# Performance work log

Measured on AMD Instinct MI355X. Metric: run time of the kernel, lower is better.

Reference implementation:

```python
import jax, jax.numpy as jnp
import numpy as np

D_MODEL, N_HEAD, D_HEAD, N_LAYERS, D_FF = 1024, 16, 64, 6, 4096
SEQ_LEN, MEM_LEN, BATCH, CLAMP_LEN = 512, 128, 4, 512
LN_EPS = 1e-5


def layernorm(x, g, b):
    mu = jnp.mean(x, axis=-1, keepdims=True)
    var = jnp.var(x, axis=-1, keepdims=True)
    return (x - mu) * jax.lax.rsqrt(var + LN_EPS) * g + b


def rel_shift(x):
    # x: (qlen, rlen, B, H) -> Transformer-XL relative shift
    q, r, b, n = x.shape
    zp = jnp.zeros((q, 1, b, n), x.dtype)
    xp = jnp.concatenate([zp, x], axis=1).reshape(r + 1, q, b, n)
    return xp[1:].reshape(q, r, b, n)


def pos_embedding(klen):
    # sinusoidal embedding on positions klen-1 .. 0, clamped at CLAMP_LEN
    pos = jnp.arange(klen - 1, -1, -1.0, dtype=jnp.float32)
    pos = jnp.minimum(pos, float(CLAMP_LEN))
    inv_freq = 1.0 / (10000.0 ** (jnp.arange(0.0, D_MODEL, 2.0) / D_MODEL))
    sin_inp = pos[:, None] * inv_freq[None, :]  # (klen, D/2)
    return jnp.concatenate([jnp.sin(sin_inp), jnp.cos(sin_inp)], axis=-1)  # (klen, D)


def setup_inputs() -> dict:
    key = jax.random.key(0)
    ks = jax.random.split(key, 16)
    s = 0.02
    return {
        "inputs": jax.random.normal(ks[0], (SEQ_LEN, BATCH, D_MODEL), jnp.float32),
        "mems": jax.random.normal(ks[1], (N_LAYERS, MEM_LEN, BATCH, D_MODEL), jnp.float32),
        "r_w_bias": jax.random.normal(ks[2], (N_HEAD, D_HEAD), jnp.float32) * s,
        "r_r_bias": jax.random.normal(ks[3], (N_HEAD, D_HEAD), jnp.float32) * s,
        "qkv_w": jax.random.normal(ks[4], (N_LAYERS, 3 * N_HEAD * D_HEAD, D_MODEL), jnp.float32) * s,
        "r_w": jax.random.normal(ks[5], (N_LAYERS, N_HEAD * D_HEAD, D_MODEL), jnp.float32) * s,
        "o_w": jax.random.normal(ks[6], (N_LAYERS, D_MODEL, N_HEAD * D_HEAD), jnp.float32) * s,
        "ln1_g": jnp.ones((N_LAYERS, D_MODEL), jnp.float32),
        "ln1_b": jnp.zeros((N_LAYERS, D_MODEL), jnp.float32),
        "ff_w1": jax.random.normal(ks[7], (N_LAYERS, D_FF, D_MODEL), jnp.float32) * s,
        "ff_b1": jnp.zeros((N_LAYERS, D_FF), jnp.float32),
        "ff_w2": jax.random.normal(ks[8], (N_LAYERS, D_MODEL, D_FF), jnp.float32) * s,
        "ff_b2": jnp.zeros((N_LAYERS, D_MODEL), jnp.float32),
        "ln2_g": jnp.ones((N_LAYERS, D_MODEL), jnp.float32),
        "ln2_b": jnp.zeros((N_LAYERS, D_MODEL), jnp.float32),
        "fin_g": jnp.ones((D_MODEL,), jnp.float32),
        "fin_b": jnp.zeros((D_MODEL,), jnp.float32),
    }


def reference(inputs, mems, r_w_bias, r_r_bias, qkv_w, r_w, o_w,
              ln1_g, ln1_b, ff_w1, ff_b1, ff_w2, ff_b2, ln2_g, ln2_b,
              fin_g, fin_b):
    qlen, bsz, _ = inputs.shape
    mlen = mems.shape[1]
    klen = mlen + qlen
    scale = 1.0 / np.sqrt(D_HEAD)

    pos_emb = pos_embedding(klen)  # (klen, D)
    # causal mask with memory: True = masked
    attn_mask = jnp.triu(jnp.ones((qlen, klen), bool), k=1 + mlen)

    x = inputs  # (T, B, D)
    for l in range(N_LAYERS):
        # ---- relative multi-head attention (pre_lnorm) ----
        cat = jnp.concatenate([mems[l], x], axis=0)           # (klen, B, D)
        h = layernorm(cat, ln1_g[l], ln1_b[l])
        w_heads = jnp.einsum('kbd,ed->kbe', h, qkv_w[l])      # (klen, B, 3HD)
        r_head_k = jnp.einsum('kd,ed->ke', pos_emb, r_w[l])   # (klen, HD)
        hd = N_HEAD * D_HEAD
        q = w_heads[-qlen:, :, :hd].reshape(qlen, bsz, N_HEAD, D_HEAD)
        k = w_heads[:, :, hd:2 * hd].reshape(klen, bsz, N_HEAD, D_HEAD)
        v = w_heads[:, :, 2 * hd:].reshape(klen, bsz, N_HEAD, D_HEAD)
        r_head_k = r_head_k.reshape(klen, N_HEAD, D_HEAD)

        AC = jnp.einsum('ibnd,jbnd->ijbn', q + r_w_bias, k)
        BD = rel_shift(jnp.einsum('ibnd,jnd->ijbn', q + r_r_bias, r_head_k))
        score = (AC + BD) * scale                              # (q, k, B, H)
        score = jnp.where(attn_mask[:, :, None, None], -jnp.inf, score)
        prob = jax.nn.softmax(score, axis=1)
        attn_vec = jnp.einsum('ijbn,jbnd->ibnd', prob, v).reshape(qlen, bsz, hd)
        attn_out = jnp.einsum('ibe,de->ibd', attn_vec, o_w[l])
        x = x + attn_out

        # ---- position-wise FFN (pre_lnorm) ----
        hf = layernorm(x, ln2_g[l], ln2_b[l])
        hf = jax.nn.relu(jnp.einsum('ibd,fd->ibf', hf, ff_w1[l]) + ff_b1[l])
        hf = jnp.einsum('ibf,df->ibd', hf, ff_w2[l]) + ff_b2[l]
        x = x + hf

    return layernorm(x, fin_g, fin_b)
```

## Files before the change

kernel.cpp:

```cpp
#include <hip/hip_runtime.h>
#include <math.h>
#include <stdint.h>

#define DM    1024
#define NH    16
#define DH    64
#define NL    6
#define DFF   4096
#define QLEN  512
#define MLEN  128
#define B_    4
#define KL    640
#define CLAMP 512
#define EPS   1e-5f

typedef _Float16 f16x8 __attribute__((ext_vector_type(8)));
typedef _Float16 f16x4 __attribute__((ext_vector_type(4)));
typedef float    f32x4 __attribute__((ext_vector_type(4)));

__device__ __forceinline__ void gload16(const void* g, void* l) {
  __builtin_amdgcn_global_load_lds(
      (const __attribute__((address_space(1))) void*)g,
      (__attribute__((address_space(3))) void*)l, 16, 0, 0);
}

__device__ __forceinline__ float block_sum(float v, float* sm4) {
#pragma unroll
  for (int o = 32; o > 0; o >>= 1) v += __shfl_down(v, o, 64);
  int lane = threadIdx.x & 63, wid = threadIdx.x >> 6;
  if (lane == 0) sm4[wid] = v;
  __syncthreads();
  float r = sm4[0] + sm4[1] + sm4[2] + sm4[3];
  __syncthreads();
  return r;
}

__global__ __launch_bounds__(256) void pos_emb_kernel(_Float16* __restrict__ pe) {
  int p = blockIdx.x;
  float pos = fminf((float)(KL - 1 - p), (float)CLAMP);
  for (int f = threadIdx.x; f < 512; f += 256) {
    float inv = powf(10000.0f, -(float)f * (1.0f / 512.0f));
    float a = pos * inv;
    pe[(size_t)p * DM + f]       = (_Float16)sinf(a);
    pe[(size_t)p * DM + 512 + f] = (_Float16)cosf(a);
  }
}

__global__ __launch_bounds__(256) void cast_w_kernel(
    const float* __restrict__ s0, const float* __restrict__ s1,
    const float* __restrict__ s2, const float* __restrict__ s3,
    const float* __restrict__ s4, _Float16* __restrict__ dst) {
  size_t i = ((size_t)blockIdx.x * 256 + threadIdx.x) * 4;
  const float* src; size_t off;
  if (i < 3145728)      { src = s0; off = 0; }
  else if (i < 4194304) { src = s1; off = 3145728; }
  else if (i < 5242880) { src = s2; off = 4194304; }
  else if (i < 9437184) { src = s3; off = 5242880; }
  else                  { src = s4; off = 9437184; }
  float4 v = *(const float4*)(src + (i - off));
  f16x4 o = { (_Float16)v.x, (_Float16)v.y, (_Float16)v.z, (_Float16)v.w };
  *(f16x4*)(dst + i) = o;
}

template <int OUTF16>
__global__ __launch_bounds__(256) void ln_kernel(
    const float* __restrict__ src0, const float* __restrict__ src1,
    const float* __restrict__ g, const float* __restrict__ b,
    float* __restrict__ outf, _Float16* __restrict__ outh, int rows0) {
  __shared__ float sm4[4];
  int row = blockIdx.x;
  const float* src = (row < rows0) ? (src0 + (size_t)row * DM)
                                   : (src1 + (size_t)(row - rows0) * DM);
  float4 v = ((const float4*)src)[threadIdx.x];
  float mean = block_sum(v.x + v.y + v.z + v.w, sm4) * (1.0f / DM);
  float dx = v.x - mean, dy = v.y - mean, dz = v.z - mean, dw = v.w - mean;
  float var = block_sum(dx * dx + dy * dy + dz * dz + dw * dw, sm4) * (1.0f / DM);
  float rstd = rsqrtf(var + EPS);
  float4 gg = ((const float4*)g)[threadIdx.x];
  float4 bb = ((const float4*)b)[threadIdx.x];
  float ox = dx * rstd * gg.x + bb.x;
  float oy = dy * rstd * gg.y + bb.y;
  float oz = dz * rstd * gg.z + bb.z;
  float ow = dw * rstd * gg.w + bb.w;
  if (OUTF16) {
    f16x4 o = { (_Float16)ox, (_Float16)oy, (_Float16)oz, (_Float16)ow };
    *(f16x4*)(outh + (size_t)row * DM + threadIdx.x * 4) = o;
  } else {
    float4 o = { ox, oy, oz, ow };
    ((float4*)(outf + (size_t)row * DM))[threadIdx.x] = o;
  }
}

template <int BIAS, int RELU, int RESID, int OUTF16>
__global__ __launch_bounds__(256) void gemm_mfma(
    const _Float16* __restrict__ A, const _Float16* __restrict__ B,
    const float* __restrict__ bias, const float* __restrict__ resid,
    float* __restrict__ Cf, _Float16* __restrict__ Ch,
    int M, int N, int K) {
  __shared__ alignas(16) _Float16 As[128 * 32];
  __shared__ alignas(16) _Float16 Bs[128 * 32];
  const int t = threadIdx.x;
  const int lane = t & 63, wid = t >> 6;
  const int m0 = blockIdx.y * 128, n0 = blockIdx.x * 128;
  const int wm = (wid >> 1) * 64, wn = (wid & 1) * 64;

  const int c0 = wid * 64 + lane, c1 = c0 + 256;
  const _Float16* Ap0 = A + (size_t)(m0 + (c0 >> 2)) * K + (c0 & 3) * 8;
  const _Float16* Ap1 = A + (size_t)(m0 + (c1 >> 2)) * K + (c1 & 3) * 8;
  const _Float16* Bp0 = B + (size_t)(n0 + (c0 >> 2)) * K + (c0 & 3) * 8;
  const _Float16* Bp1 = B + (size_t)(n0 + (c1 >> 2)) * K + (c1 & 3) * 8;
  _Float16* Asw0 = &As[wid * 512];
  _Float16* Asw1 = &As[wid * 512 + 2048];
  _Float16* Bsw0 = &Bs[wid * 512];
  _Float16* Bsw1 = &Bs[wid * 512 + 2048];

  f32x4 acc[4][4] = {};
  for (int k0 = 0; k0 < K; k0 += 32) {
    __syncthreads();
    gload16(Ap0 + k0, Asw0);
    gload16(Ap1 + k0, Asw1);
    gload16(Bp0 + k0, Bsw0);
    gload16(Bp1 + k0, Bsw1);
    __syncthreads();
    f16x8 af[4], bf[4];
#pragma unroll
    for (int f = 0; f < 4; ++f) {
      af[f] = *(const f16x8*)&As[(wm + f * 16 + (lane & 15)) * 32 + (lane >> 4) * 8];
      bf[f] = *(const f16x8*)&Bs[(wn + f * 16 + (lane & 15)) * 32 + (lane >> 4) * 8];
    }
#pragma unroll
    for (int i = 0; i < 4; ++i)
#pragma unroll
      for (int j = 0; j < 4; ++j)
        acc[i][j] = __builtin_amdgcn_mfma_f32_16x16x32_f16(af[i], bf[j], acc[i][j], 0, 0, 0);
  }
#pragma unroll
  for (int i = 0; i < 4; ++i) {
#pragma unroll
    for (int j = 0; j < 4; ++j) {
      const int n = n0 + wn + j * 16 + (lane & 15);
      float bv = 0.0f;
      if (BIAS) bv = bias[n];
#pragma unroll
      for (int r = 0; r < 4; ++r) {
        const int m = m0 + wm + i * 16 + (lane >> 4) * 4 + r;
        float v = acc[i][j][r] + bv;
        if (RELU) v = fmaxf(v, 0.0f);
        if (RESID) v += resid[(size_t)m * N + n];
        if (OUTF16) Ch[(size_t)m * N + n] = (_Float16)v;
        else        Cf[(size_t)m * N + n] = v;
      }
    }
  }
}

__global__ __launch_bounds__(256) void gemm_sk(
    const _Float16* __restrict__ A, const _Float16* __restrict__ B,
    _Float16* __restrict__ pk, int M, int N, int K, int Ks) {
  __shared__ alignas(16) _Float16 As[128 * 32];
  __shared__ alignas(16) _Float16 Bs[128 * 32];
  const int t = threadIdx.x;
  const int lane = t & 63, wid = t >> 6;
  const int m0 = blockIdx.y * 128, n0 = blockIdx.x * 128;
  const int z = blockIdx.z;
  const int kbase = z * Ks;
  const int wm = (wid >> 1) * 64, wn = (wid & 1) * 64;

  const int c0 = wid * 64 + lane, c1 = c0 + 256;
  const _Float16* Ap0 = A + (size_t)(m0 + (c0 >> 2)) * K + kbase + (c0 & 3) * 8;
  const _Float16* Ap1 = A + (size_t)(m0 + (c1 >> 2)) * K + kbase + (c1 & 3) * 8;
  const _Float16* Bp0 = B + (size_t)(n0 + (c0 >> 2)) * K + kbase + (c0 & 3) * 8;
  const _Float16* Bp1 = B + (size_t)(n0 + (c1 >> 2)) * K + kbase + (c1 & 3) * 8;
  _Float16* Asw0 = &As[wid * 512];
  _Float16* Asw1 = &As[wid * 512 + 2048];
  _Float16* Bsw0 = &Bs[wid * 512];
  _Float16* Bsw1 = &Bs[wid * 512 + 2048];

  f32x4 acc[4][4] = {};
  for (int k0 = 0; k0 < Ks; k0 += 32) {
    __syncthreads();
    gload16(Ap0 + k0, Asw0);
    gload16(Ap1 + k0, Asw1);
    gload16(Bp0 + k0, Bsw0);
    gload16(Bp1 + k0, Bsw1);
    __syncthreads();
    f16x8 af[4], bf[4];
#pragma unroll
    for (int f = 0; f < 4; ++f) {
      af[f] = *(const f16x8*)&As[(wm + f * 16 + (lane & 15)) * 32 + (lane >> 4) * 8];
      bf[f] = *(const f16x8*)&Bs[(wn + f * 16 + (lane & 15)) * 32 + (lane >> 4) * 8];
    }
#pragma unroll
    for (int i = 0; i < 4; ++i)
#pragma unroll
      for (int j = 0; j < 4; ++j)
        acc[i][j] = __builtin_amdgcn_mfma_f32_16x16x32_f16(af[i], bf[j], acc[i][j], 0, 0, 0);
  }
  _Float16* out = pk + (size_t)z * M * N;
#pragma unroll
  for (int i = 0; i < 4; ++i)
#pragma unroll
    for (int j = 0; j < 4; ++j) {
      const int n = n0 + wn + j * 16 + (lane & 15);
#pragma unroll
      for (int r = 0; r < 4; ++r) {
        const int m = m0 + wm + i * 16 + (lane >> 4) * 4 + r;
        out[(size_t)m * N + n] = (_Float16)acc[i][j][r];
      }
    }
}

template <int SK, int BIAS, int RELU, int RESID, int OUTF16>
__global__ __launch_bounds__(256) void reduce_k(
    const _Float16* __restrict__ pk, const float* __restrict__ bias,
    const float* __restrict__ resid, float* __restrict__ Cf,
    _Float16* __restrict__ Ch, int MN, int Nmask) {
  const int idx = (blockIdx.x * 256 + threadIdx.x) * 8;
  float s[8] = {};
#pragma unroll
  for (int zz = 0; zz < SK; ++zz) {
    f16x8 v = *(const f16x8*)(pk + (size_t)zz * MN + idx);
#pragma unroll
    for (int e = 0; e < 8; ++e) s[e] += (float)v[e];
  }
  if (BIAS) {
    const int n0 = idx & Nmask;
#pragma unroll
    for (int e = 0; e < 8; ++e) s[e] += bias[n0 + e];
  }
  if (RELU)
#pragma unroll
    for (int e = 0; e < 8; ++e) s[e] = fmaxf(s[e], 0.0f);
  if (RESID) {
    float4 r0 = *(const float4*)(resid + idx);
    float4 r1 = *(const float4*)(resid + idx + 4);
    s[0] += r0.x; s[1] += r0.y; s[2] += r0.z; s[3] += r0.w;
    s[4] += r1.x; s[5] += r1.y; s[6] += r1.z; s[7] += r1.w;
  }
  if (OUTF16) {
    f16x8 o;
#pragma unroll
    for (int e = 0; e < 8; ++e) o[e] = (_Float16)s[e];
    *(f16x8*)(Ch + idx) = o;
  } else {
    float4 o0 = { s[0], s[1], s[2], s[3] };
    float4 o1 = { s[4], s[5], s[6], s[7] };
    *(float4*)(Cf + idx) = o0;
    *(float4*)(Cf + idx + 4) = o1;
  }
}

__global__ __launch_bounds__(256, 4) void attn_kernel(
    const _Float16* __restrict__ wh,
    const _Float16* __restrict__ rk,
    const float* __restrict__ rwb,
    const float* __restrict__ rrb,
    _Float16* __restrict__ po,
    float* __restrict__ pm,
    float* __restrict__ pl) {
  __shared__ alignas(16) _Float16 RR[128 * 72];
  __shared__ alignas(16) _Float16 KS[64 * 72];
  __shared__ alignas(16) _Float16 QS[64 * 72];

  const int i0 = blockIdx.x * 64, n = blockIdx.y;
  const int b = blockIdx.z & 3, zz = blockIdx.z >> 2;
  const int t = threadIdx.x, lane = t & 63, wid = t >> 6;
  const int g = lane >> 4, li = lane & 15;
  const int strip = wid * 16;

  f16x8 qw[2], qr[2];
#pragma unroll
  for (int ks_ = 0; ks_ < 2; ++ks_) {
    const _Float16* qp =
        wh + ((size_t)(MLEN + i0 + strip + li) * B_ + b) * 3072 + n * 64 + ks_ * 32 + g * 8;
    f16x8 qv = *(const f16x8*)qp;
#pragma unroll
    for (int e = 0; e < 8; ++e) {
      float f0 = (float)qv[e];
      qw[ks_][e] = (_Float16)(f0 + rwb[n * 64 + ks_ * 32 + g * 8 + e]);
      qr[ks_][e] = (_Float16)(f0 + rrb[n * 64 + ks_ * 32 + g * 8 + e]);
    }
  }

  f32x4 o_[4] = {};
  float mrun[4], lrun[4];
#pragma unroll
  for (int r = 0; r < 4; ++r) { mrun[r] = -INFINITY; lrun[r] = 0.0f; }

  const float SC = 0.125f * 1.44269504f;
  const int ntiles = i0 / 64 + 3;
  for (int tt = zz; tt < ntiles; tt += 2) {
    const int j0 = tt * 64;
    __syncthreads();
    {
      int row = t >> 2, c = (t & 3) * 16;
      const _Float16* kp = wh + ((size_t)(j0 + row) * B_ + b) * 3072 + 1024 + n * 64 + c;
      *(f16x8*)&KS[row * 72 + c] = *(const f16x8*)kp;
      *(f16x8*)&KS[row * 72 + c + 8] = *(const f16x8*)(kp + 8);
    }
    {
      int row = t >> 1, c = (t & 1) * 32;
      int mrow = j0 - i0 + 448 + row;
      if (mrow > KL - 1) mrow = KL - 1;
      const _Float16* rp = rk + (size_t)mrow * DM + n * 64 + c;
#pragma unroll
      for (int cc = 0; cc < 32; cc += 8)
        *(f16x8*)&RR[row * 72 + c + cc] = *(const f16x8*)(rp + cc);
    }
    __syncthreads();
    f32x4 acs[4] = {};
#pragma unroll
    for (int ks_ = 0; ks_ < 2; ++ks_)
#pragma unroll
      for (int cf = 0; cf < 4; ++cf) {
        f16x8 bk = *(const f16x8*)&KS[(cf * 16 + li) * 72 + ks_ * 32 + g * 8];
        acs[cf] = __builtin_amdgcn_mfma_f32_16x16x32_f16(qw[ks_], bk, acs[cf], 0, 0, 0);
      }
#pragma unroll
    for (int half = 0; half < 2; ++half) {
      f32x4 acq[4] = {};
#pragma unroll
      for (int ks_ = 0; ks_ < 2; ++ks_)
#pragma unroll
        for (int cf = 0; cf < 4; ++cf) {
          f16x8 br = *(const f16x8*)&RR[((half * 4 + cf) * 16 + li) * 72 + ks_ * 32 + g * 8];
          acq[cf] = __builtin_amdgcn_mfma_f32_16x16x32_f16(qr[ks_], br, acq[cf], 0, 0, 0);
        }
#pragma unroll
      for (int cf = 0; cf < 4; ++cf)
#pragma unroll
        for (int r = 0; r < 4; ++r) {
          int il = strip + g * 4 + r;
          int jl = (half * 4 + cf) * 16 + li - 63 + il;
          if ((unsigned)jl < 64u) QS[il * 72 + jl] = (_Float16)acq[cf][r];
        }
    }
    __syncthreads();
    float pf[4][4], fac[4];
#pragma unroll
    for (int r = 0; r < 4; ++r) {
      int il = strip + g * 4 + r, gi = i0 + il;
      float sv[4], mx = -INFINITY;
#pragma unroll
      for (int cf = 0; cf < 4; ++cf) {
        int jl = cf * 16 + li;
        float v = (acs[cf][r] + (float)QS[il * 72 + jl]) * SC;
        if (j0 + jl > gi + MLEN) v = -INFINITY;
        sv[cf] = v;
        mx = fmaxf(mx, v);
      }
#pragma unroll
      for (int o2 = 1; o2 < 16; o2 <<= 1) mx = fmaxf(mx, __shfl_xor(mx, o2, 64));
      float mnew = fmaxf(mrun[r], mx);
      float fc = exp2f(mrun[r] - mnew);
      float sum = 0.0f;
#pragma unroll
      for (int cf = 0; cf < 4; ++cf) { pf[cf][r] = exp2f(sv[cf] - mnew); sum += pf[cf][r]; }
#pragma unroll
      for (int o2 = 1; o2 < 16; o2 <<= 1) sum += __shfl_xor(sum, o2, 64);
      lrun[r] = lrun[r] * fc + sum;
      mrun[r] = mnew;
      fac[r] = fc;
    }
    __syncthreads();
#pragma unroll
    for (int cf = 0; cf < 4; ++cf)
#pragma unroll
      for (int r = 0; r < 4; ++r)
        QS[(strip + g * 4 + r) * 72 + cf * 16 + li] = (_Float16)pf[cf][r];
#pragma unroll
    for (int it = 0; it < 2; ++it) {
      int j = t & 63, d0 = (t >> 6) * 8 + it * 32;
      f16x8 vv = *(const f16x8*)(wh + ((size_t)(j0 + j) * B_ + b) * 3072 + 2048 + n * 64 + d0);
#pragma unroll
      for (int e = 0; e < 8; ++e) KS[(d0 + e) * 72 + j] = vv[e];
    }
    __syncthreads();
#pragma unroll
    for (int cf = 0; cf < 4; ++cf)
#pragma unroll
      for (int r = 0; r < 4; ++r)
        o_[cf][r] *= fac[r];
#pragma unroll
    for (int ks_ = 0; ks_ < 2; ++ks_) {
      f16x8 pa = *(const f16x8*)&QS[(strip + li) * 72 + ks_ * 32 + g * 8];
#pragma unroll
      for (int cf = 0; cf < 4; ++cf) {
        f16x8 bv = *(const f16x8*)&KS[(cf * 16 + li) * 72 + ks_ * 32 + g * 8];
        o_[cf] = __builtin_amdgcn_mfma_f32_16x16x32_f16(pa, bv, o_[cf], 0, 0, 0);
      }
    }
  }
  const size_t obase = (size_t)zz * (QLEN * B_ * 1024);
#pragma unroll
  for (int cf = 0; cf < 4; ++cf)
#pragma unroll
    for (int r = 0; r < 4; ++r) {
      int row = strip + g * 4 + r;
      float l = lrun[r];
      float oo = (l > 0.0f) ? o_[cf][r] / l : 0.0f;
      po[obase + ((size_t)(i0 + row) * B_ + b) * 1024 + n * 64 + cf * 16 + li] = (_Float16)oo;
    }
  if (li == 0) {
#pragma unroll
    for (int r = 0; r < 4; ++r) {
      int row = strip + g * 4 + r;
      int idx = ((i0 + row) * B_ + b) * 16 + n;
      pm[zz * 32768 + idx] = (lrun[r] > 0.0f) ? mrun[r] : -3.0e38f;
      pl[zz * 32768 + idx] = lrun[r];
    }
  }
}

__global__ __launch_bounds__(256) void attn_combine(
    const _Float16* __restrict__ po, const float* __restrict__ pm,
    const float* __restrict__ pl, _Float16* __restrict__ av) {
  const size_t e = ((size_t)blockIdx.x * 256 + threadIdx.x) * 8;
  const int mlidx = (int)(e >> 10) * 16 + (((int)e & 1023) >> 6);
  float m1 = pm[mlidx], m2 = pm[32768 + mlidx];
  float l1 = pl[mlidx], l2 = pl[32768 + mlidx];
  float M = fmaxf(m1, m2);
  float w1 = l1 * exp2f(m1 - M), w2 = l2 * exp2f(m2 - M);
  float inv = 1.0f / (w1 + w2);
  w1 *= inv; w2 *= inv;
  f16x8 o1 = *(const f16x8*)(po + e);
  f16x8 o2 = *(const f16x8*)(po + 2097152 + e);
  f16x8 o;
#pragma unroll
  for (int k = 0; k < 8; ++k) o[k] = (_Float16)(w1 * (float)o1[k] + w2 * (float)o2[k]);
  *(f16x8*)(av + e) = o;
}

extern "C" void kernel_launch(void* const* d_in, const int* in_sizes, int n_in,
                              void* d_out, int out_size, void* d_ws, size_t ws_size,
                              hipStream_t stream) {
  const float* inputs = (const float*)d_in[0];
  const float* mems   = (const float*)d_in[1];
  const float* rwb    = (const float*)d_in[2];
  const float* rrb    = (const float*)d_in[3];
  const float* qkv_w  = (const float*)d_in[4];
  const float* r_w    = (const float*)d_in[5];
  const float* o_w    = (const float*)d_in[6];
  const float* ln1_g  = (const float*)d_in[7];
  const float* ln1_b  = (const float*)d_in[8];
  const float* ff_w1  = (const float*)d_in[9];
  const float* ff_b1  = (const float*)d_in[10];
  const float* ff_w2  = (const float*)d_in[11];
  const float* ff_b2  = (const float*)d_in[12];
  const float* ln2_g  = (const float*)d_in[13];
  const float* ln2_b  = (const float*)d_in[14];
  const float* fin_g  = (const float*)d_in[15];
  const float* fin_b  = (const float*)d_in[16];
  float* out = (float*)d_out;

  float* ws = (float*)d_ws;
  float* xbuf = ws;
  _Float16* fb = (_Float16*)(ws + 2097152);
  _Float16* wh_h  = fb;
  _Float16* rk_h  = wh_h + 7864320;
  _Float16* pe_h  = rk_h + 655360;
  _Float16* h_h   = pe_h + 655360;
  _Float16* av_h  = h_h + 2621440;
  _Float16* ffh_h = av_h + 2097152;
  _Float16* wb_h  = ffh_h + 8388608;
  _Float16* wq = wb_h;
  _Float16* wr = wb_h + 3145728;
  _Float16* wo = wb_h + 4194304;
  _Float16* w1 = wb_h + 5242880;
  _Float16* w2 = wb_h + 9437184;
  _Float16* pk_big = wh_h;
  _Float16* pk_rk  = ffh_h;
  _Float16* po     = ffh_h;
  float*    pm     = (float*)(ffh_h + 4194304);
  float*    pl     = pm + 65536;

  pos_emb_kernel<<<KL, 256, 0, stream>>>(pe_h);

  const float* xcur = inputs;
  for (int l = 0; l < NL; ++l) {
    cast_w_kernel<<<13312, 256, 0, stream>>>(
        qkv_w + (size_t)l * 3145728, r_w + (size_t)l * 1048576,
        o_w + (size_t)l * 1048576, ff_w1 + (size_t)l * 4194304,
        ff_w2 + (size_t)l * 4194304, wb_h);
    ln_kernel<1><<<KL * B_, 256, 0, stream>>>(
        mems + (size_t)l * MLEN * B_ * DM, xcur,
        ln1_g + l * DM, ln1_b + l * DM, nullptr, h_h, MLEN * B_);
    gemm_mfma<0, 0, 0, 1><<<dim3(3072 / 128, 2560 / 128), 256, 0, stream>>>(
        h_h, wq, nullptr, nullptr, nullptr, wh_h, 2560, 3072, DM);
    gemm_sk<<<dim3(DM / 128, KL / 128, 8), 256, 0, stream>>>(
        pe_h, wr, pk_rk, KL, DM, DM, DM / 8);
    reduce_k<8, 0, 0, 0, 1><<<KL * DM / 2048, 256, 0, stream>>>(
        pk_rk, nullptr, nullptr, nullptr, rk_h, KL * DM, DM - 1);
    attn_kernel<<<dim3(QLEN / 64, NH, B_ * 2), 256, 0, stream>>>(
        wh_h, rk_h, rwb, rrb, po, pm, pl);
    attn_combine<<<1024, 256, 0, stream>>>(po, pm, pl, av_h);
    gemm_sk<<<dim3(DM / 128, (QLEN * B_) / 128, 4), 256, 0, stream>>>(
        av_h, wo, pk_big, QLEN * B_, DM, DM, DM / 4);
    reduce_k<4, 0, 0, 1, 0><<<QLEN * B_ * DM / 2048, 256, 0, stream>>>(
        pk_big, nullptr, xcur, xbuf, nullptr, QLEN * B_ * DM, DM - 1);
    ln_kernel<1><<<QLEN * B_, 256, 0, stream>>>(
        xbuf, nullptr, ln2_g + l * DM, ln2_b + l * DM, nullptr, h_h, 1 << 30);
    gemm_mfma<1, 1, 0, 1><<<dim3(DFF / 128, (QLEN * B_) / 128), 256, 0, stream>>>(
        h_h, w1, ff_b1 + (size_t)l * DFF, nullptr, nullptr, ffh_h, QLEN * B_, DFF, DM);
    gemm_sk<<<dim3(DM / 128, (QLEN * B_) / 128, 4), 256, 0, stream>>>(
        ffh_h, w2, pk_big, QLEN * B_, DM, DFF, DFF / 4);
    reduce_k<4, 1, 0, 1, 0><<<QLEN * B_ * DM / 2048, 256, 0, stream>>>(
        pk_big, ff_b2 + (size_t)l * DM, xbuf, xbuf, nullptr, QLEN * B_ * DM, DM - 1);
    xcur = xbuf;
  }
  ln_kernel<0><<<QLEN * B_, 256, 0, stream>>>(xbuf, nullptr, fin_g, fin_b, out, nullptr, 1 << 30);
}
```

Baseline: 1.227 ms.

## Batch weight casts and r_head_k GEMM across layers; cut attention barriers

All layer weights are now cast to fp16 in one launch up front, and the position projection r_head_k for all six layers is computed in a single wide GEMM before the layer loop. This replaces the per-layer cast, split-k GEMM and reduce launches. The attention kernel gives V its own transposed shared buffer loaded together with K, and gives each wave a private score/probability strip. That removes two block-wide barriers per tile, at the cost of more shared memory and lower occupancy (launch bound 4 to 3). Workspace use grows considerably to hold all fp16 weights and all per-layer r_head_k at once.

```diff
diff --git a/kernel.cpp b/kernel.cpp
--- a/kernel.cpp
+++ b/kernel.cpp
@@ -46,20 +46,26 @@
   }
 }
 
-__global__ __launch_bounds__(256) void cast_w_kernel(
-    const float* __restrict__ s0, const float* __restrict__ s1,
-    const float* __restrict__ s2, const float* __restrict__ s3,
-    const float* __restrict__ s4, _Float16* __restrict__ dst) {
-  size_t i = ((size_t)blockIdx.x * 256 + threadIdx.x) * 4;
-  const float* src; size_t off;
-  if (i < 3145728)      { src = s0; off = 0; }
-  else if (i < 4194304) { src = s1; off = 3145728; }
-  else if (i < 5242880) { src = s2; off = 4194304; }
-  else if (i < 9437184) { src = s3; off = 5242880; }
-  else                  { src = s4; off = 9437184; }
-  float4 v = *(const float4*)(src + (i - off));
-  f16x4 o = { (_Float16)v.x, (_Float16)v.y, (_Float16)v.z, (_Float16)v.w };
-  *(f16x4*)(dst + i) = o;
+__global__ __launch_bounds__(256) void cast_all_kernel(
+    const float* __restrict__ qkv, const float* __restrict__ rw,
+    const float* __restrict__ ow, const float* __restrict__ f1,
+    const float* __restrict__ f2,
+    _Float16* __restrict__ dq, _Float16* __restrict__ dr,
+    _Float16* __restrict__ dow, _Float16* __restrict__ d1,
+    _Float16* __restrict__ d2) {
+  size_t i = ((size_t)blockIdx.x * 256 + threadIdx.x) * 8;
+  const float* s; _Float16* d; size_t off;
+  if (i < 18874368)      { s = qkv; d = dq;  off = 0; }
+  else if (i < 25165824) { s = rw;  d = dr;  off = 18874368; }
+  else if (i < 31457280) { s = ow;  d = dow; off = 25165824; }
+  else if (i < 56623104) { s = f1;  d = d1;  off = 31457280; }
+  else                   { s = f2;  d = d2;  off = 56623104; }
+  size_t k = i - off;
+  float4 a = *(const float4*)(s + k);
+  float4 b = *(const float4*)(s + k + 4);
+  f16x8 o = { (_Float16)a.x, (_Float16)a.y, (_Float16)a.z, (_Float16)a.w,
+              (_Float16)b.x, (_Float16)b.y, (_Float16)b.z, (_Float16)b.w };
+  *(f16x8*)(d + k) = o;
 }
 
 template <int OUTF16>
@@ -250,7 +256,7 @@
   }
 }
 
-__global__ __launch_bounds__(256, 4) void attn_kernel(
+__global__ __launch_bounds__(256, 3) void attn_kernel(
     const _Float16* __restrict__ wh,
     const _Float16* __restrict__ rk,
     const float* __restrict__ rwb,
@@ -258,15 +264,17 @@
     _Float16* __restrict__ po,
     float* __restrict__ pm,
     float* __restrict__ pl) {
+  __shared__ alignas(16) _Float16 KS[64 * 72];
+  __shared__ alignas(16) _Float16 VT[64 * 72];
   __shared__ alignas(16) _Float16 RR[128 * 72];
-  __shared__ alignas(16) _Float16 KS[64 * 72];
-  __shared__ alignas(16) _Float16 QS[64 * 72];
+  __shared__ alignas(16) _Float16 QS[4][16 * 72];
 
   const int i0 = blockIdx.x * 64, n = blockIdx.y;
   const int b = blockIdx.z & 3, zz = blockIdx.z >> 2;
   const int t = threadIdx.x, lane = t & 63, wid = t >> 6;
   const int g = lane >> 4, li = lane & 15;
   const int strip = wid * 16;
+  _Float16* QSw = QS[wid];
 
   f16x8 qw[2], qr[2];
 #pragma unroll
@@ -298,11 +306,18 @@
       *(f16x8*)&KS[row * 72 + c] = *(const f16x8*)kp;
       *(f16x8*)&KS[row * 72 + c + 8] = *(const f16x8*)(kp + 8);
     }
+#pragma unroll
+    for (int it = 0; it < 2; ++it) {
+      int j = t & 63, d0 = (t >> 6) * 8 + it * 32;
+      f16x8 vv = *(const f16x8*)(wh + ((size_t)(j0 + j) * B_ + b) * 3072 + 2048 + n * 64 + d0);
+#pragma unroll
+      for (int e = 0; e < 8; ++e) VT[(d0 + e) * 72 + j] = vv[e];
+    }
     {
       int row = t >> 1, c = (t & 1) * 32;
       int mrow = j0 - i0 + 448 + row;
       if (mrow > KL - 1) mrow = KL - 1;
-      const _Float16* rp = rk + (size_t)mrow * DM + n * 64 + c;
+      const _Float16* rp = rk + (size_t)mrow * 6144 + n * 64 + c;
 #pragma unroll
       for (int cc = 0; cc < 32; cc += 8)
         *(f16x8*)&RR[row * 72 + c + cc] = *(const f16x8*)(rp + cc);
@@ -332,10 +347,9 @@
         for (int r = 0; r < 4; ++r) {
           int il = strip + g * 4 + r;
           int jl = (half * 4 + cf) * 16 + li - 63 + il;
-          if ((unsigned)jl < 64u) QS[il * 72 + jl] = (_Float16)acq[cf][r];
+          if ((unsigned)jl < 64u) QSw[(g * 4 + r) * 72 + jl] = (_Float16)acq[cf][r];
         }
     }
-    __syncthreads();
     float pf[4][4], fac[4];
 #pragma unroll
     for (int r = 0; r < 4; ++r) {
@@ -344,7 +358,7 @@
 #pragma unroll
       for (int cf = 0; cf < 4; ++cf) {
         int jl = cf * 16 + li;
-        float v = (acs[cf][r] + (float)QS[il * 72 + jl]) * SC;
+        float v = (acs[cf][r] + (float)QSw[(g * 4 + r) * 72 + jl]) * SC;
         if (j0 + jl > gi + MLEN) v = -INFINITY;
         sv[cf] = v;
         mx = fmaxf(mx, v);
@@ -362,20 +376,11 @@
       mrun[r] = mnew;
       fac[r] = fc;
     }
-    __syncthreads();
 #pragma unroll
     for (int cf = 0; cf < 4; ++cf)
 #pragma unroll
       for (int r = 0; r < 4; ++r)
-        QS[(strip + g * 4 + r) * 72 + cf * 16 + li] = (_Float16)pf[cf][r];
-#pragma unroll
-    for (int it = 0; it < 2; ++it) {
-      int j = t & 63, d0 = (t >> 6) * 8 + it * 32;
-      f16x8 vv = *(const f16x8*)(wh + ((size_t)(j0 + j) * B_ + b) * 3072 + 2048 + n * 64 + d0);
-#pragma unroll
-      for (int e = 0; e < 8; ++e) KS[(d0 + e) * 72 + j] = vv[e];
-    }
-    __syncthreads();
+        QSw[(g * 4 + r) * 72 + cf * 16 + li] = (_Float16)pf[cf][r];
 #pragma unroll
     for (int cf = 0; cf < 4; ++cf)
 #pragma unroll
@@ -383,10 +388,10 @@
         o_[cf][r] *= fac[r];
 #pragma unroll
     for (int ks_ = 0; ks_ < 2; ++ks_) {
-      f16x8 pa = *(const f16x8*)&QS[(strip + li) * 72 + ks_ * 32 + g * 8];
+      f16x8 pa = *(const f16x8*)&QSw[li * 72 + ks_ * 32 + g * 8];
 #pragma unroll
       for (int cf = 0; cf < 4; ++cf) {
-        f16x8 bv = *(const f16x8*)&KS[(cf * 16 + li) * 72 + ks_ * 32 + g * 8];
+        f16x8 bv = *(const f16x8*)&VT[(cf * 16 + li) * 72 + ks_ * 32 + g * 8];
         o_[cf] = __builtin_amdgcn_mfma_f32_16x16x32_f16(pa, bv, o_[cf], 0, 0, 0);
       }
     }
@@ -456,56 +461,53 @@
   float* ws = (float*)d_ws;
   float* xbuf = ws;
   _Float16* fb = (_Float16*)(ws + 2097152);
-  _Float16* wh_h  = fb;
-  _Float16* rk_h  = wh_h + 7864320;
-  _Float16* pe_h  = rk_h + 655360;
-  _Float16* h_h   = pe_h + 655360;
-  _Float16* av_h  = h_h + 2621440;
-  _Float16* ffh_h = av_h + 2097152;
-  _Float16* wb_h  = ffh_h + 8388608;
-  _Float16* wq = wb_h;
-  _Float16* wr = wb_h + 3145728;
-  _Float16* wo = wb_h + 4194304;
-  _Float16* w1 = wb_h + 5242880;
-  _Float16* w2 = wb_h + 9437184;
-  _Float16* pk_big = wh_h;
-  _Float16* pk_rk  = ffh_h;
-  _Float16* po     = ffh_h;
-  float*    pm     = (float*)(ffh_h + 4194304);
+  _Float16* wh_h   = fb;
+  _Float16* rk_all = wh_h + 7864320;
+  _Float16* pe_h   = rk_all + 3932160;
+  _Float16* h_h    = pe_h + 655360;
+  _Float16* av_h   = h_h + 2621440;
+  _Float16* ffh_h  = av_h + 2097152;
+  _Float16* pk     = ffh_h + 8388608;
+  _Float16* po     = pk + 8388608;
+  float*    pm     = (float*)(po + 4194304);
   float*    pl     = pm + 65536;
+  _Float16* wq_all = (_Float16*)(pl + 65536);
+  _Float16* rw_all = wq_all + 18874368;
+  _Float16* wo_all = rw_all + 6291456;
+  _Float16* w1_all = wo_all + 6291456;
+  _Float16* w2_all = w1_all + 25165824;
 
   pos_emb_kernel<<<KL, 256, 0, stream>>>(pe_h);
+  cast_all_kernel<<<39936, 256, 0, stream>>>(
+      qkv_w, r_w, o_w, ff_w1, ff_w2, wq_all, rw_all, wo_all, w1_all, w2_all);
+  gemm_sk<<<dim3(6144 / 128, 640 / 128, 2), 256, 0, stream>>>(
+      pe_h, rw_all, pk, KL, 6144, DM, DM / 2);
+  reduce_k<2, 0, 0, 0, 1><<<KL * 6144 / 2048, 256, 0, stream>>>(
+      pk, nullptr, nullptr, nullptr, rk_all, KL * 6144, 0);
 
   const float* xcur = inputs;
   for (int l = 0; l < NL; ++l) {
-    cast_w_kernel<<<13312, 256, 0, stream>>>(
-        qkv_w + (size_t)l * 3145728, r_w + (size_t)l * 1048576,
-        o_w + (size_t)l * 1048576, ff_w1 + (size_t)l * 4194304,
-        ff_w2 + (size_t)l * 4194304, wb_h);
     ln_kernel<1><<<KL * B_, 256, 0, stream>>>(
         mems + (size_t)l * MLEN * B_ * DM, xcur,
         ln1_g + l * DM, ln1_b + l * DM, nullptr, h_h, MLEN * B_);
     gemm_mfma<0, 0, 0, 1><<<dim3(3072 / 128, 2560 / 128), 256, 0, stream>>>(
-        h_h, wq, nullptr, nullptr, nullptr, wh_h, 2560, 3072, DM);
-    gemm_sk<<<dim3(DM / 128, KL / 128, 8), 256, 0, stream>>>(
-        pe_h, wr, pk_rk, KL, DM, DM, DM / 8);
-    reduce_k<8, 0, 0, 0, 1><<<KL * DM / 2048, 256, 0, stream>>>(
-        pk_rk, nullptr, nullptr, nullptr, rk_h, KL * DM, DM - 1);
+        h_h, wq_all + (size_t)l * 3145728, nullptr, nullptr, nullptr, wh_h, 2560, 3072, DM);
     attn_kernel<<<dim3(QLEN / 64, NH, B_ * 2), 256, 0, stream>>>(
-        wh_h, rk_h, rwb, rrb, po, pm, pl);
+        wh_h, rk_all + (size_t)l * 1024, rwb, rrb, po, pm, pl);
     attn_combine<<<1024, 256, 0, stream>>>(po, pm, pl, av_h);
     gemm_sk<<<dim3(DM / 128, (QLEN * B_) / 128, 4), 256, 0, stream>>>(
-        av_h, wo, pk_big, QLEN * B_, DM, DM, DM / 4);
+        av_h, wo_all + (size_t)l * 1048576, pk, QLEN * B_, DM, DM, DM / 4);
     reduce_k<4, 0, 0, 1, 0><<<QLEN * B_ * DM / 2048, 256, 0, stream>>>(
-        pk_big, nullptr, xcur, xbuf, nullptr, QLEN * B_ * DM, DM - 1);
+        pk, nullptr, xcur, xbuf, nullptr, QLEN * B_ * DM, DM - 1);
     ln_kernel<1><<<QLEN * B_, 256, 0, stream>>>(
         xbuf, nullptr, ln2_g + l * DM, ln2_b + l * DM, nullptr, h_h, 1 << 30);
     gemm_mfma<1, 1, 0, 1><<<dim3(DFF / 128, (QLEN * B_) / 128), 256, 0, stream>>>(
-        h_h, w1, ff_b1 + (size_t)l * DFF, nullptr, nullptr, ffh_h, QLEN * B_, DFF, DM);
+        h_h, w1_all + (size_t)l * 4194304, ff_b1 + (size_t)l * DFF, nullptr,
+        nullptr, ffh_h, QLEN * B_, DFF, DM);
     gemm_sk<<<dim3(DM / 128, (QLEN * B_) / 128, 4), 256, 0, stream>>>(
-        ffh_h, w2, pk_big, QLEN * B_, DM, DFF, DFF / 4);
+        ffh_h, w2_all + (size_t)l * 4194304, pk, QLEN * B_, DM, DFF, DFF / 4);
     reduce_k<4, 1, 0, 1, 0><<<QLEN * B_ * DM / 2048, 256, 0, stream>>>(
-        pk_big, ff_b2 + (size_t)l * DM, xbuf, xbuf, nullptr, QLEN * B_ * DM, DM - 1);
+        pk, ff_b2 + (size_t)l * DM, xbuf, xbuf, nullptr, QLEN * B_ * DM, DM - 1);
     xcur = xbuf;
   }
   ln_kernel<0><<<QLEN * B_, 256, 0, stream>>>(xbuf, nullptr, fin_g, fin_b, out, nullptr, 1 << 30);
```

Measured after the change: 1.237 ms. No clear change (+0.8%).
